# Optimization experiments

Measured on AMD Instinct MI355X. Metric: run time of the kernel, lower is better.

The kernel has to match this reference:

```python
import jax, jax.numpy as jnp
import numpy as np

EPS = 1.1920929e-07  # float32 eps, matches torch.finfo(torch.float32).eps
QMAX = 127.0         # 2**(8-1)-1 for 8-bit symmetric quantization
NUM_HEADS = 12


def _round_ste(x):
    return x + jax.lax.stop_gradient(jnp.round(x) - x)


def _floor_ste(x):
    return x + jax.lax.stop_gradient(jnp.floor(x) - x)


def _act_quant(x):
    # per-tensor symmetric 8-bit (QuantAct + SymmetricQuantFunction)
    s = jax.lax.stop_gradient(jnp.maximum(jnp.max(jnp.abs(x)) / QMAX, EPS))
    return jnp.clip(_round_ste(x / s), -QMAX - 1.0, QMAX), s


def _weight_quant(w):
    # per-output-channel symmetric 8-bit (scale.view(-1,1) path in linear_quantize)
    s = jax.lax.stop_gradient(jnp.maximum(jnp.max(jnp.abs(w), axis=1) / QMAX, EPS))
    return jnp.clip(_round_ste(w / s[:, None]), -QMAX - 1.0, QMAX), s


def _fixedpoint_requant(pre_act, pre_s, z_s):
    # fixedpoint_mul: requantize int accumulator (value pre_act on scale pre_s)
    # onto scale z_s using a 31-bit mantissa/exponent decomposition (batch_frexp).
    def int_path(pa):
        z_int = jnp.round(pa / pre_s)
        ns = pre_s / z_s
        e = jnp.floor(jnp.log2(ns)) + 1.0          # frexp exponent: ns = m * 2**e, m in [0.5,1)
        m = jnp.floor(ns * jnp.exp2(-e) * 2.0 ** 31 + 0.5)  # ROUND_HALF_UP mantissa * 2**31
        out = jnp.round(z_int * m * jnp.exp2(e - 31.0))
        return jnp.clip(out, -QMAX - 1.0, QMAX)
    hard = jax.lax.stop_gradient(int_path(pre_act))
    soft = pre_act / z_s                            # STE backward: grad / z_scaling_factor
    return soft + jax.lax.stop_gradient(hard - soft)


def _int_softmax(x_int, sf, output_bit=8, n=15):
    # IntSoftmax (shiftmax) with int_exp_shift; x_int = logits / sf (integer-valued)
    x_int = x_int - jnp.max(x_int, axis=-1, keepdims=True)
    x_int = x_int + _floor_ste(x_int / 2.0) - _floor_ste(x_int / 16.0)
    x0 = jax.lax.stop_gradient(jnp.floor(-1.0 / sf))
    x_int = jnp.maximum(x_int, n * x0)
    q = _floor_ste(x_int / x0)
    r = x_int - x0 * q
    exp_int = jnp.clip(_floor_ste((r / 2.0 - x0) * jnp.exp2(n - q)), 0.0, None)
    esum = jnp.minimum(jnp.sum(exp_int, axis=-1, keepdims=True), 2.0 ** 31 - 1.0)
    factor = _floor_ste((2.0 ** 31 - 1.0) / esum)
    exp_int = _floor_ste(exp_int * factor / 2.0 ** (31 - output_bit + 1))
    return exp_int, 1.0 / 2.0 ** (output_bit - 1)


def setup_inputs() -> dict:
    key = jax.random.key(0)
    k1, k2, k3, k4, k5 = jax.random.split(key, 5)
    B, N, C = 8, 577, 768
    return {
        "x": jax.random.normal(k1, (B, N, C), dtype=jnp.float32),
        "w_qkv": jax.random.normal(k2, (3 * C, C), dtype=jnp.float32) * 0.02,
        "b_qkv": jax.random.normal(k3, (3 * C,), dtype=jnp.float32) * 0.01,
        "w_proj": jax.random.normal(k4, (C, C), dtype=jnp.float32) * 0.02,
        "b_proj": jax.random.normal(k5, (C,), dtype=jnp.float32) * 0.01,
    }


def reference(x, w_qkv, b_qkv, w_proj, b_proj):
    B, N, C = x.shape
    H = NUM_HEADS
    D = C // H
    # ---- quantize input activation and qkv weight, integer GEMM ----
    x_int, s_x = _act_quant(x)                         # [B,N,C] int-valued, scalar scale
    wq_int, s_wq = _weight_quant(w_qkv)                # [3C,C], per-channel scale [3C]
    acc_s = s_x * s_wq                                 # accumulator scale [3C]
    qkv_int = jnp.einsum('bnc,oc->bno', x_int, wq_int) + _round_ste(b_qkv / acc_s)
    qkv_f = qkv_int * acc_s                            # dequantized qkv [B,N,3C]
    # ---- requantize qkv to per-tensor 8-bit via fixed-point mul ----
    s_qkv = jax.lax.stop_gradient(jnp.maximum(jnp.max(jnp.abs(qkv_f)) / QMAX, EPS))
    qkv8 = _fixedpoint_requant(qkv_f, acc_s, s_qkv)    # int8-valued [B,N,3C]
    qkv8 = qkv8.reshape(B, N, 3, H, D).transpose(2, 0, 3, 1, 4)
    q, k, v = qkv8[0], qkv8[1], qkv8[2]                # each [B,H,N,D]
    # ---- integer attention logits; float scale carries head_dim**-0.5 ----
    attn_int = jnp.einsum('bhnd,bhmd->bhnm', q, k)
    s_attn = s_qkv * s_qkv * (D ** -0.5)
    sm_int, s_sm = _int_softmax(attn_int, s_attn)      # int probs on scale 1/128
    # ---- integer attn @ v ----
    ctx_int = jnp.einsum('bhnm,bhmd->bhnd', sm_int, v)
    ctx_f = (ctx_int * (s_sm * s_qkv)).transpose(0, 2, 1, 3).reshape(B, N, C)
    s_ctx = jax.lax.stop_gradient(jnp.maximum(jnp.max(jnp.abs(ctx_f)) / QMAX, EPS))
    ctx8 = _fixedpoint_requant(ctx_f, s_sm * s_qkv, s_ctx)
    # ---- quantized output projection ----
    wp_int, s_wp = _weight_quant(w_proj)
    out_s = s_ctx * s_wp
    out_int = jnp.einsum('bnc,oc->bno', ctx8, wp_int) + _round_ste(b_proj / out_s)
    return out_int * out_s
```

## Files before the change

### kernel.cpp

```cpp
#include <hip/hip_runtime.h>
#include <math.h>

#define BQ 8
#define SEQ 577
#define CH 768
#define NH 12
#define HD 64
#define M_ROWS (BQ * SEQ)
#define QKV_CH (3 * CH)
#define NX (M_ROWS * CH)
#define EPSF 1.1920929e-07f
#define F2P31 2147483648.0f

#define VT_ROW 640
#define P_STRIDE 688

#define NSLOT 64
#define SLOT_STRIDE 16

typedef __attribute__((ext_vector_type(4))) int i32x4;

__device__ __forceinline__ float slot_scale(const unsigned* __restrict__ s) {
  float m = 0.f;
#pragma unroll
  for (int i = 0; i < NSLOT; ++i) m = fmaxf(m, __uint_as_float(s[i * SLOT_STRIDE]));
  return fmaxf(m / 127.0f, EPSF);
}

__device__ __forceinline__ void mfma_gemm_core_lds(
    const signed char* __restrict__ A, const signed char* __restrict__ Bm,
    signed char* As, signed char* Bs,
    int arow0, int bcol0, int w, int lane, i32x4 acc[4][4]) {
  int c = lane & 15, q = lane >> 4;
  int lr = lane >> 2;
  int ksb = (lane & 3) << 4;
  const signed char* Aw = As + ((w & 1) << 12);
  const signed char* Bw = Bs + ((w >> 1) << 12);
  for (int k0 = 0; k0 < CH; k0 += 64) {
#pragma unroll
    for (int u = 0; u < 2; ++u) {
      int row = (w << 5) + (u << 4) + lr;
      __builtin_amdgcn_global_load_lds(
          (const __attribute__((address_space(1))) void*)(A + (size_t)(arow0 + row) * CH + k0 + ksb),
          (__attribute__((address_space(3))) void*)(As + (w << 11) + (u << 10)),
          16, 0, 0);
      __builtin_amdgcn_global_load_lds(
          (const __attribute__((address_space(1))) void*)(Bm + (size_t)(bcol0 + row) * CH + k0 + ksb),
          (__attribute__((address_space(3))) void*)(Bs + (w << 11) + (u << 10)),
          16, 0, 0);
    }
    __syncthreads();
    i32x4 af[4], bf[4];
#pragma unroll
    for (int i = 0; i < 4; ++i)
      af[i] = *(const i32x4*)(Aw + (((i << 4) + c) << 6) + (q << 4));
#pragma unroll
    for (int j = 0; j < 4; ++j)
      bf[j] = *(const i32x4*)(Bw + (((j << 4) + c) << 6) + (q << 4));
#pragma unroll
    for (int i = 0; i < 4; ++i)
#pragma unroll
      for (int j = 0; j < 4; ++j)
        acc[i][j] = __builtin_amdgcn_mfma_i32_16x16x64_i8(af[i], bf[j], acc[i][j], 0, 0, 0);
    __syncthreads();
  }
}

__global__ __launch_bounds__(256) void k_prep(
    const float* __restrict__ x, const float* __restrict__ w_qkv,
    const float* __restrict__ w_proj,
    signed char* __restrict__ WQ8, float* __restrict__ SWQ,
    signed char* __restrict__ WP8, float* __restrict__ SWP,
    unsigned* __restrict__ mxx) {
  __shared__ float red[4];
  int blk = blockIdx.x, tid = threadIdx.x;
  if (blk < QKV_CH + CH) {
    const float* wr; signed char* w8; float* sw; int r;
    if (blk < QKV_CH) { r = blk; wr = w_qkv + (size_t)r * CH; w8 = WQ8 + (size_t)r * CH; sw = SWQ; }
    else { r = blk - QKV_CH; wr = w_proj + (size_t)r * CH; w8 = WP8 + (size_t)r * CH; sw = SWP; }
    const float4* wr4 = (const float4*)wr;
    float4 v = {0.f, 0.f, 0.f, 0.f};
    float m = 0.f;
    if (tid < CH / 4) {
      v = wr4[tid];
      m = fmaxf(fmaxf(fabsf(v.x), fabsf(v.y)), fmaxf(fabsf(v.z), fabsf(v.w)));
    }
#pragma unroll
    for (int o = 32; o; o >>= 1) m = fmaxf(m, __shfl_xor(m, o, 64));
    if ((tid & 63) == 0) red[tid >> 6] = m;
    __syncthreads();
    float mm = fmaxf(fmaxf(red[0], red[1]), fmaxf(red[2], red[3]));
    float s = fmaxf(mm / 127.0f, EPSF);
    if (tid == 0) sw[r] = s;
    if (tid < CH / 4) {
      int pk = 0;
#pragma unroll
      for (int u = 0; u < 4; ++u) {
        float xv = (u == 0) ? v.x : (u == 1) ? v.y : (u == 2) ? v.z : v.w;
        float q = rintf(xv / s);
        q = fminf(fmaxf(q, -128.f), 127.f);
        pk |= ((int)(signed char)q & 0xff) << (u * 8);
      }
      ((int*)w8)[tid] = pk;
    }
  } else {
    int ab = blk - (QKV_CH + CH);
    const float4* x4 = (const float4*)x;
    float m = 0.f;
    for (int i = ab * 256 + tid; i < NX / 4; i += 1024 * 256) {
      float4 v = x4[i];
      m = fmaxf(m, fmaxf(fmaxf(fabsf(v.x), fabsf(v.y)), fmaxf(fabsf(v.z), fabsf(v.w))));
    }
#pragma unroll
    for (int o = 32; o; o >>= 1) m = fmaxf(m, __shfl_xor(m, o, 64));
    if ((tid & 63) == 0) red[tid >> 6] = m;
    __syncthreads();
    if (tid == 0)
      atomicMax(&mxx[(ab & (NSLOT - 1)) * SLOT_STRIDE],
                __float_as_uint(fmaxf(fmaxf(red[0], red[1]), fmaxf(red[2], red[3]))));
  }
}

__global__ void k_aquant(const float* __restrict__ x, int n,
                         const unsigned* __restrict__ mxx, signed char* __restrict__ x8) {
  float s = slot_scale(mxx);
  int n4 = n >> 2;
  const float4* x4 = (const float4*)x;
  int* dst = (int*)x8;
  int stride = gridDim.x * blockDim.x;
  for (int i = blockIdx.x * blockDim.x + threadIdx.x; i < n4; i += stride) {
    float4 v = x4[i];
    int pk = 0;
#pragma unroll
    for (int u = 0; u < 4; ++u) {
      float xv = (u == 0) ? v.x : (u == 1) ? v.y : (u == 2) ? v.z : v.w;
      float q = rintf(xv / s);
      q = fminf(fmaxf(q, -128.f), 127.f);
      pk |= ((int)(signed char)q & 0xff) << (u * 8);
    }
    dst[i] = pk;
  }
}

__global__ __launch_bounds__(256) void k_gemm_qkv(
    const signed char* __restrict__ A, const signed char* __restrict__ Bm,
    const float* __restrict__ swq, const float* __restrict__ bias,
    const unsigned* __restrict__ mxx, int* __restrict__ Cq, unsigned* __restrict__ mxq) {
  __shared__ __align__(16) signed char As[8192], Bs[8192];
  __shared__ float red[4];
  int t = threadIdx.x;
  int lane = t & 63, w = t >> 6;
  int c = lane & 15, q = lane >> 4;
  int arow = blockIdx.y * 128 + (w & 1) * 64;
  int bcol = blockIdx.x * 128 + (w >> 1) * 64;
  i32x4 acc[4][4] = {};
  mfma_gemm_core_lds(A, Bm, As, Bs, blockIdx.y * 128, blockIdx.x * 128, w, lane, acc);
  float s_x = slot_scale(mxx);
  float lmax = 0.f;
#pragma unroll
  for (int j = 0; j < 4; ++j) {
    int ccol = bcol + j * 16 + c;
    float accs = s_x * swq[ccol];
    int bint = (int)rintf(bias[ccol] / accs);
#pragma unroll
    for (int i = 0; i < 4; ++i)
#pragma unroll
      for (int r = 0; r < 4; ++r) {
        int rr = arow + i * 16 + q * 4 + r;
        if (rr < M_ROWS) {
          int qv = acc[i][j][r] + bint;
          Cq[(size_t)rr * QKV_CH + ccol] = qv;
          lmax = fmaxf(lmax, fabsf((float)qv * accs));
        }
      }
  }
#pragma unroll
  for (int off = 32; off; off >>= 1) lmax = fmaxf(lmax, __shfl_xor(lmax, off, 64));
  if (lane == 0) red[w] = lmax;
  __syncthreads();
  if (t == 0)
    atomicMax(&mxq[((blockIdx.y * 18 + blockIdx.x) & (NSLOT - 1)) * SLOT_STRIDE],
              __float_as_uint(fmaxf(fmaxf(red[0], red[1]), fmaxf(red[2], red[3]))));
}

#define QK_BLKS 870
__global__ __launch_bounds__(256) void k_qkv_requant(
    const int* __restrict__ Cq, const float* __restrict__ swq,
    const unsigned* __restrict__ mxx, const unsigned* __restrict__ mxq,
    signed char* __restrict__ Q8, signed char* __restrict__ K8,
    signed char* __restrict__ VT8) {
  float s_x = slot_scale(mxx);
  float s_qkv = slot_scale(mxq);
  int blk = blockIdx.x, tid = threadIdx.x;
  if (blk < QK_BLKS) {
    int bx = blk % 6, by = blk / 6;
    int o = bx * 256 + tid;
    float accs = s_x * swq[o];
    float ns = accs / s_qkv;
    int e; float f = frexpf(ns, &e);
    float mm = floorf(f * F2P31 + 0.5f);
    float pw = __int_as_float((e + 96) << 23);
    int isK = (o >= CH);
    int rem = o - (isK ? CH : 0);
    int h = rem >> 6, d = rem & 63;
    signed char* dstb = isK ? K8 : Q8;
    int bn0 = by * 32;
    int bnend = min(bn0 + 32, M_ROWS);
    for (int bn = bn0; bn < bnend; ++bn) {
      int qv = Cq[(size_t)bn * QKV_CH + o];
      float qf = (float)qv * accs;
      float z = rintf(qf / accs);
      float t8 = rintf((z * mm) * pw);
      t8 = fminf(fmaxf(t8, -128.f), 127.f);
      int b = bn / SEQ, n = bn - b * SEQ;
      dstb[(((size_t)(b * NH + h) * SEQ + n) << 6) + d] = (signed char)t8;
    }
  } else {
    __shared__ __align__(16) signed char VTt[64 * 68];
    int vt = blk - QK_BLKS;
    int bh = vt / 10, n0 = (vt - bh * 10) * 64;
    int b = bh / NH, h = bh - b * NH;
    int od = tid & 63;
    int o = 2 * CH + h * 64 + od;
    float accs = s_x * swq[o];
    float ns = accs / s_qkv;
    int e; float f = frexpf(ns, &e);
    float mm = floorf(f * F2P31 + 0.5f);
    float pw = __int_as_float((e + 96) << 23);
    int nr = tid >> 6;
    for (int p = 0; p < 16; ++p) {
      int nl = nr * 16 + p;
      int n = n0 + nl;
      signed char v = 0;
      if (n < SEQ) {
        int qv = Cq[(size_t)(b * SEQ + n) * QKV_CH + o];
        float qf = (float)qv * accs;
        float z = rintf(qf / accs);
        float t8 = rintf((z * mm) * pw);
        t8 = fminf(fmaxf(t8, -128.f), 127.f);
        v = (signed char)t8;
      }
      VTt[od * 68 + nl] = v;
    }
    __syncthreads();
    int w16 = tid & 15, dr = tid >> 4;
#pragma unroll
    for (int pp = 0; pp < 4; ++pp) {
      int d = pp * 16 + dr;
      int val = *(const int*)&VTt[d * 68 + w16 * 4];
      *(int*)(VT8 + (size_t)bh * (64 * VT_ROW) + (size_t)d * VT_ROW + n0 + w16 * 4) = val;
    }
  }
}

__global__ __launch_bounds__(256, 6) void k_attn(
    const signed char* __restrict__ Q8, const signed char* __restrict__ K8,
    const signed char* __restrict__ VT8, const unsigned* __restrict__ mxq,
    int* __restrict__ ctxi, unsigned* __restrict__ mxc) {
  __shared__ __align__(16) unsigned char P[16 * P_STRIDE];
  __shared__ int Rmax[4][16];
  __shared__ unsigned long long Rsum[4][16];
  __shared__ float Rav[4];
  int tid = threadIdx.x;
  int t = tid & 63, wid = tid >> 6;
  int lin = blockIdx.x;
  int j = lin >> 3;
  int bh = (lin & 7) * 12 + j / 37;
  int qt = j % 37;
  int b = bh / NH, h = bh - b * NH;
  int col = t & 15, q4 = t >> 4;
  const signed char* Qb = Q8 + (((size_t)bh * SEQ + qt * 16 + col) << 6);
  i32x4 qa = *(const i32x4*)(Qb + q4 * 16);
  const signed char* Kb = K8 + ((size_t)bh * SEQ << 6);
  int kt0 = wid * 10;
  i32x4 sv[10];
  bool vld[10];
  int mx[4] = {-2147483647 - 1, -2147483647 - 1, -2147483647 - 1, -2147483647 - 1};
#pragma unroll
  for (int u = 0; u < 10; ++u) {
    int kt = kt0 + u;
    int krow = min(kt * 16 + col, SEQ - 1);
    const signed char* kr = Kb + ((size_t)krow << 6);
    i32x4 kb = *(const i32x4*)(kr + q4 * 16);
    i32x4 a = {0, 0, 0, 0};
    a = __builtin_amdgcn_mfma_i32_16x16x64_i8(qa, kb, a, 0, 0, 0);
    sv[u] = a;
    bool valid = (kt < 36) | ((kt == 36) & (col < 1));
    vld[u] = valid;
#pragma unroll
    for (int r = 0; r < 4; ++r)
      if (valid) mx[r] = max(mx[r], a[r]);
  }
#pragma unroll
  for (int r = 0; r < 4; ++r) {
    mx[r] = max(mx[r], __shfl_xor(mx[r], 1, 64));
    mx[r] = max(mx[r], __shfl_xor(mx[r], 2, 64));
    mx[r] = max(mx[r], __shfl_xor(mx[r], 4, 64));
    mx[r] = max(mx[r], __shfl_xor(mx[r], 8, 64));
  }
  if (col == 0) {
#pragma unroll
    for (int r = 0; r < 4; ++r) Rmax[wid][q4 * 4 + r] = mx[r];
  }
  __syncthreads();
#pragma unroll
  for (int r = 0; r < 4; ++r) {
    int row = q4 * 4 + r;
    mx[r] = max(max(Rmax[0][row], Rmax[1][row]), max(Rmax[2][row], Rmax[3][row]));
  }
  float s_qkv = slot_scale(mxq);
  float s_attn = (s_qkv * s_qkv) * 0.125f;
  float x0f = floorf(-1.0f / s_attn);
  int x0i = (int)x0f;
  int bi = -x0i;
  int nx0i = 15 * x0i;
  int twob = bi << 1;
  unsigned Mq = 0xFFFFFFFFu / (unsigned)bi + 1u;
  bool bOne = (Mq == 0u);
  unsigned long long su[4] = {0ull, 0ull, 0ull, 0ull};
#pragma unroll
  for (int u = 0; u < 10; ++u) {
#pragma unroll
    for (int r = 0; r < 4; ++r) {
      int d = sv[u][r] - mx[r];
      int xi = d + (d >> 1) - (d >> 4);
      xi = max(xi, nx0i);
      xi = min(xi, 0);
      unsigned a = (unsigned)(-xi);
      unsigned q = bOne ? a : __umulhi(a, Mq);
      int rr = (int)(a - q * (unsigned)bi);
      unsigned m = (unsigned)(twob - rr);
      unsigned ue = (m << 15) >> (q + 1);
      ue = vld[u] ? ue : 0u;
      su[r] += ue;
      sv[u][r] = (int)ue;
    }
  }
#pragma unroll
  for (int r = 0; r < 4; ++r) {
    su[r] += __shfl_xor(su[r], 1, 64);
    su[r] += __shfl_xor(su[r], 2, 64);
    su[r] += __shfl_xor(su[r], 4, 64);
    su[r] += __shfl_xor(su[r], 8, 64);
  }
  if (col == 0) {
#pragma unroll
    for (int r = 0; r < 4; ++r) Rsum[wid][q4 * 4 + r] = su[r];
  }
  __syncthreads();
  float facS[4];
#pragma unroll
  for (int r = 0; r < 4; ++r) {
    int row = q4 * 4 + r;
    unsigned long long dv = ((Rsum[0][row] + Rsum[1][row]) + Rsum[2][row]) + Rsum[3][row];
    float esum = fminf((float)dv, F2P31);
    facS[r] = floorf(F2P31 / esum) * 5.9604644775390625e-08f;
  }
#pragma unroll
  for (int u = 0; u < 10; ++u) {
    int kt = kt0 + u;
#pragma unroll
    for (int r = 0; r < 4; ++r) {
      float e = (float)(unsigned)sv[u][r];
      int p = (int)floorf(e * facS[r]);
      P[(q4 * 4 + r) * P_STRIDE + kt * 16 + col] = (unsigned char)p;
    }
  }
  __syncthreads();
  const signed char* Vb = VT8 + (size_t)bh * (64 * VT_ROW);
  i32x4 ac0 = {0, 0, 0, 0}, ac1 = {0, 0, 0, 0};
#pragma unroll
  for (int mc = 0; mc < 10; mc += 2) {
    i32x4 pa0 = *(const i32x4*)&P[col * P_STRIDE + mc * 64 + q4 * 16];
    i32x4 vb0 = *(const i32x4*)(Vb + (size_t)(wid * 16 + col) * VT_ROW + mc * 64 + q4 * 16);
    ac0 = __builtin_amdgcn_mfma_i32_16x16x64_i8(pa0, vb0, ac0, 0, 0, 0);
    i32x4 pa1 = *(const i32x4*)&P[col * P_STRIDE + (mc + 1) * 64 + q4 * 16];
    i32x4 vb1 = *(const i32x4*)(Vb + (size_t)(wid * 16 + col) * VT_ROW + (mc + 1) * 64 + q4 * 16);
    ac1 = __builtin_amdgcn_mfma_i32_16x16x64_i8(pa1, vb1, ac1, 0, 0, 0);
  }
  float pre_s = 0.0078125f * s_qkv;
  float avmax = 0.f;
#pragma unroll
  for (int r = 0; r < 4; ++r) {
    int n = qt * 16 + q4 * 4 + r;
    if (n < SEQ) {
      int cacc = ac0[r] + ac1[r];
      ctxi[((size_t)(b * SEQ + n)) * CH + h * 64 + wid * 16 + col] = cacc;
      avmax = fmaxf(avmax, fabsf((float)cacc * pre_s));
    }
  }
#pragma unroll
  for (int off = 32; off; off >>= 1) avmax = fmaxf(avmax, __shfl_xor(avmax, off, 64));
  if (t == 0) Rav[wid] = avmax;
  __syncthreads();
  if (tid == 0)
    atomicMax(&mxc[(blockIdx.x & (NSLOT - 1)) * SLOT_STRIDE],
              __float_as_uint(fmaxf(fmaxf(Rav[0], Rav[1]), fmaxf(Rav[2], Rav[3]))));
}

__global__ void k_ctx_requant(const int* __restrict__ ctxi, const unsigned* __restrict__ mxq,
                              const unsigned* __restrict__ mxc, signed char* __restrict__ C8) {
  float s_qkv = slot_scale(mxq);
  float pre_s = 0.0078125f * s_qkv;
  float s_ctx = slot_scale(mxc);
  float ns = pre_s / s_ctx;
  int e;
  float f = frexpf(ns, &e);
  float mm = floorf(f * F2P31 + 0.5f);
  float pw = exp2f((float)e - 31.0f);
  int total4 = (M_ROWS * CH) / 4;
  int stride = gridDim.x * blockDim.x;
  const int4* src = (const int4*)ctxi;
  int* dst = (int*)C8;
  for (int i = blockIdx.x * blockDim.x + threadIdx.x; i < total4; i += stride) {
    int4 v = src[i];
    int pk = 0;
#pragma unroll
    for (int u = 0; u < 4; ++u) {
      int cv = (u == 0) ? v.x : (u == 1) ? v.y : (u == 2) ? v.z : v.w;
      float cf = (float)cv * pre_s;
      float z = rintf(cf / pre_s);
      float t8 = rintf((z * mm) * pw);
      t8 = fminf(fmaxf(t8, -128.f), 127.f);
      pk |= ((int)(signed char)t8 & 0xff) << (u * 8);
    }
    dst[i] = pk;
  }
}

__global__ __launch_bounds__(256) void k_gemm_out(
    const signed char* __restrict__ A, const signed char* __restrict__ Bm,
    const float* __restrict__ swp, const float* __restrict__ bias,
    const unsigned* __restrict__ mxc, float* __restrict__ outp) {
  __shared__ __align__(16) signed char As[8192], Bs[8192];
  int t = threadIdx.x;
  int lane = t & 63, w = t >> 6;
  int c = lane & 15, q = lane >> 4;
  int arow = blockIdx.y * 128 + (w & 1) * 64;
  int bcol = blockIdx.x * 128 + (w >> 1) * 64;
  i32x4 acc[4][4] = {};
  mfma_gemm_core_lds(A, Bm, As, Bs, blockIdx.y * 128, blockIdx.x * 128, w, lane, acc);
  float s_ctx = slot_scale(mxc);
#pragma unroll
  for (int j = 0; j < 4; ++j) {
    int ccol = bcol + j * 16 + c;
    float outs = s_ctx * swp[ccol];
    int bint = (int)rintf(bias[ccol] / outs);
#pragma unroll
    for (int i = 0; i < 4; ++i)
#pragma unroll
      for (int r = 0; r < 4; ++r) {
        int rr = arow + i * 16 + q * 4 + r;
        if (rr < M_ROWS)
          outp[(size_t)rr * CH + ccol] = (float)(acc[i][j][r] + bint) * outs;
      }
  }
}

extern "C" void kernel_launch(void* const* d_in, const int* in_sizes, int n_in,
                              void* d_out, int out_size, void* d_ws, size_t ws_size,
                              hipStream_t stream) {
  const float* x = (const float*)d_in[0];
  const float* w_qkv = (const float*)d_in[1];
  const float* b_qkv = (const float*)d_in[2];
  const float* w_proj = (const float*)d_in[3];
  const float* b_proj = (const float*)d_in[4];
  float* outp = (float*)d_out;

  char* ws = (char*)d_ws;
  size_t off = 0;
  auto alloc = [&](size_t sz) -> char* {
    char* p = ws + off;
    off = (off + sz + 4095) & ~(size_t)4095;
    return p;
  };
  unsigned* mxx = (unsigned*)alloc(3 * NSLOT * SLOT_STRIDE * 4);
  unsigned* mxq = mxx + NSLOT * SLOT_STRIDE;
  unsigned* mxc = mxq + NSLOT * SLOT_STRIDE;
  float* SWQ = (float*)alloc(QKV_CH * 4);
  float* SWP = (float*)alloc(CH * 4);
  signed char* WQ8 = (signed char*)alloc((size_t)QKV_CH * CH);
  signed char* WP8 = (signed char*)alloc((size_t)CH * CH);
  signed char* X8  = (signed char*)alloc((size_t)(M_ROWS + 128) * CH);
  signed char* Q8  = (signed char*)alloc((size_t)M_ROWS * CH);
  signed char* K8  = (signed char*)alloc((size_t)M_ROWS * CH);
  signed char* VT8 = (signed char*)alloc((size_t)BQ * NH * 64 * VT_ROW);
  signed char* C8  = (signed char*)alloc((size_t)(M_ROWS + 128) * CH);
  int* QKVI = (int*)alloc((size_t)M_ROWS * QKV_CH * 4);
  int* CTXI = (int*)alloc((size_t)M_ROWS * CH * 4);
  (void)ws_size;

  hipMemsetAsync(mxx, 0, 3 * NSLOT * SLOT_STRIDE * 4, stream);
  k_prep<<<QKV_CH + CH + 1024, 256, 0, stream>>>(x, w_qkv, w_proj, WQ8, SWQ, WP8, SWP, mxx);
  k_aquant<<<2048, 256, 0, stream>>>(x, NX, mxx, X8);
  dim3 g1(QKV_CH / 128, (M_ROWS + 127) / 128);
  k_gemm_qkv<<<g1, 256, 0, stream>>>(X8, WQ8, SWQ, b_qkv, mxx, QKVI, mxq);
  k_qkv_requant<<<QK_BLKS + BQ * NH * 10, 256, 0, stream>>>(QKVI, SWQ, mxx, mxq, Q8, K8, VT8);
  k_attn<<<37 * BQ * NH, 256, 0, stream>>>(Q8, K8, VT8, mxq, CTXI, mxc);
  k_ctx_requant<<<1024, 256, 0, stream>>>(CTXI, mxq, mxc, C8);
  dim3 g2(CH / 128, (M_ROWS + 127) / 128);
  k_gemm_out<<<g2, 256, 0, stream>>>(C8, WP8, SWP, b_proj, mxc, outp);
}
```

Baseline: 232.9 us.

## Fuse context requantization into output-projection GEMM A-tile loading

Removes the standalone k_ctx_requant kernel and the int8 C8 buffer. The output GEMM now reads int32 context accumulators directly, requantizes them to int8 in registers and writes them into LDS, while weights are still loaded via global_load_lds. This saves one launch and one full write and reread of the int8 buffer, but the GEMM reads A tiles as int32 (4x the bytes), and each of the 6 column blocks repeats the requant arithmetic. It also lowers the k_attn launch-bounds occupancy hint from 6 to 4.

```diff
diff --git a/kernel.cpp b/kernel.cpp
--- a/kernel.cpp
+++ b/kernel.cpp
@@ -253,7 +253,7 @@
   }
 }
 
-__global__ __launch_bounds__(256, 6) void k_attn(
+__global__ __launch_bounds__(256, 4) void k_attn(
     const signed char* __restrict__ Q8, const signed char* __restrict__ K8,
     const signed char* __restrict__ VT8, const unsigned* __restrict__ mxq,
     int* __restrict__ ctxi, unsigned* __restrict__ mxc) {
@@ -398,8 +398,20 @@
               __float_as_uint(fmaxf(fmaxf(Rav[0], Rav[1]), fmaxf(Rav[2], Rav[3]))));
 }
 
-__global__ void k_ctx_requant(const int* __restrict__ ctxi, const unsigned* __restrict__ mxq,
-                              const unsigned* __restrict__ mxc, signed char* __restrict__ C8) {
+__global__ __launch_bounds__(256) void k_gemm_out(
+    const int* __restrict__ CTXI, const signed char* __restrict__ Bm,
+    const float* __restrict__ swp, const float* __restrict__ bias,
+    const unsigned* __restrict__ mxq, const unsigned* __restrict__ mxc,
+    float* __restrict__ outp) {
+  __shared__ __align__(16) signed char As[8192], Bs[8192];
+  int t = threadIdx.x;
+  int lane = t & 63, w = t >> 6;
+  int c = lane & 15, q = lane >> 4;
+  int lr = lane >> 2;
+  int ksb = (lane & 3) << 4;
+  int arow0 = blockIdx.y * 128, bcol0 = blockIdx.x * 128;
+  int arow = arow0 + (w & 1) * 64;
+  int bcol = bcol0 + (w >> 1) * 64;
   float s_qkv = slot_scale(mxq);
   float pre_s = 0.0078125f * s_qkv;
   float s_ctx = slot_scale(mxc);
@@ -408,39 +420,51 @@
   float f = frexpf(ns, &e);
   float mm = floorf(f * F2P31 + 0.5f);
   float pw = exp2f((float)e - 31.0f);
-  int total4 = (M_ROWS * CH) / 4;
-  int stride = gridDim.x * blockDim.x;
-  const int4* src = (const int4*)ctxi;
-  int* dst = (int*)C8;
-  for (int i = blockIdx.x * blockDim.x + threadIdx.x; i < total4; i += stride) {
-    int4 v = src[i];
-    int pk = 0;
-#pragma unroll
-    for (int u = 0; u < 4; ++u) {
-      int cv = (u == 0) ? v.x : (u == 1) ? v.y : (u == 2) ? v.z : v.w;
-      float cf = (float)cv * pre_s;
-      float z = rintf(cf / pre_s);
-      float t8 = rintf((z * mm) * pw);
-      t8 = fminf(fmaxf(t8, -128.f), 127.f);
-      pk |= ((int)(signed char)t8 & 0xff) << (u * 8);
-    }
-    dst[i] = pk;
-  }
-}
-
-__global__ __launch_bounds__(256) void k_gemm_out(
-    const signed char* __restrict__ A, const signed char* __restrict__ Bm,
-    const float* __restrict__ swp, const float* __restrict__ bias,
-    const unsigned* __restrict__ mxc, float* __restrict__ outp) {
-  __shared__ __align__(16) signed char As[8192], Bs[8192];
-  int t = threadIdx.x;
-  int lane = t & 63, w = t >> 6;
-  int c = lane & 15, q = lane >> 4;
-  int arow = blockIdx.y * 128 + (w & 1) * 64;
-  int bcol = blockIdx.x * 128 + (w >> 1) * 64;
+  const signed char* Aw = As + ((w & 1) << 12);
+  const signed char* Bw = Bs + ((w >> 1) << 12);
   i32x4 acc[4][4] = {};
-  mfma_gemm_core_lds(A, Bm, As, Bs, blockIdx.y * 128, blockIdx.x * 128, w, lane, acc);
-  float s_ctx = slot_scale(mxc);
+  for (int k0 = 0; k0 < CH; k0 += 64) {
+#pragma unroll
+    for (int u = 0; u < 2; ++u) {
+      int row = (w << 5) + (u << 4) + lr;
+      __builtin_amdgcn_global_load_lds(
+          (const __attribute__((address_space(1))) void*)(Bm + (size_t)(bcol0 + row) * CH + k0 + ksb),
+          (__attribute__((address_space(3))) void*)(Bs + (w << 11) + (u << 10)),
+          16, 0, 0);
+      const int4* src = (const int4*)(CTXI + (size_t)(arow0 + row) * CH + k0 + (lane & 3) * 16);
+      int pk[4];
+#pragma unroll
+      for (int g = 0; g < 4; ++g) {
+        int4 v = src[g];
+        int p = 0;
+#pragma unroll
+        for (int uu = 0; uu < 4; ++uu) {
+          int cv = (uu == 0) ? v.x : (uu == 1) ? v.y : (uu == 2) ? v.z : v.w;
+          float cf = (float)cv * pre_s;
+          float z = rintf(cf / pre_s);
+          float t8 = rintf((z * mm) * pw);
+          t8 = fminf(fmaxf(t8, -128.f), 127.f);
+          p |= ((int)(signed char)t8 & 0xff) << (uu * 8);
+        }
+        pk[g] = p;
+      }
+      *(i32x4*)(As + (w << 11) + (u << 10) + lane * 16) = *(const i32x4*)pk;
+    }
+    __syncthreads();
+    i32x4 af[4], bf[4];
+#pragma unroll
+    for (int i = 0; i < 4; ++i)
+      af[i] = *(const i32x4*)(Aw + (((i << 4) + c) << 6) + (q << 4));
+#pragma unroll
+    for (int j = 0; j < 4; ++j)
+      bf[j] = *(const i32x4*)(Bw + (((j << 4) + c) << 6) + (q << 4));
+#pragma unroll
+    for (int i = 0; i < 4; ++i)
+#pragma unroll
+      for (int j = 0; j < 4; ++j)
+        acc[i][j] = __builtin_amdgcn_mfma_i32_16x16x64_i8(af[i], bf[j], acc[i][j], 0, 0, 0);
+    __syncthreads();
+  }
 #pragma unroll
   for (int j = 0; j < 4; ++j) {
     int ccol = bcol + j * 16 + c;
@@ -485,9 +509,8 @@
   signed char* Q8  = (signed char*)alloc((size_t)M_ROWS * CH);
   signed char* K8  = (signed char*)alloc((size_t)M_ROWS * CH);
   signed char* VT8 = (signed char*)alloc((size_t)BQ * NH * 64 * VT_ROW);
-  signed char* C8  = (signed char*)alloc((size_t)(M_ROWS + 128) * CH);
   int* QKVI = (int*)alloc((size_t)M_ROWS * QKV_CH * 4);
-  int* CTXI = (int*)alloc((size_t)M_ROWS * CH * 4);
+  int* CTXI = (int*)alloc((size_t)(M_ROWS + 128) * CH * 4);
   (void)ws_size;
 
   hipMemsetAsync(mxx, 0, 3 * NSLOT * SLOT_STRIDE * 4, stream);
@@ -497,7 +520,6 @@
   k_gemm_qkv<<<g1, 256, 0, stream>>>(X8, WQ8, SWQ, b_qkv, mxx, QKVI, mxq);
   k_qkv_requant<<<QK_BLKS + BQ * NH * 10, 256, 0, stream>>>(QKVI, SWQ, mxx, mxq, Q8, K8, VT8);
   k_attn<<<37 * BQ * NH, 256, 0, stream>>>(Q8, K8, VT8, mxq, CTXI, mxc);
-  k_ctx_requant<<<1024, 256, 0, stream>>>(CTXI, mxq, mxc, C8);
   dim3 g2(CH / 128, (M_ROWS + 127) / 128);
-  k_gemm_out<<<g2, 256, 0, stream>>>(C8, WP8, SWP, b_proj, mxc, outp);
-}
+  k_gemm_out<<<g2, 256, 0, stream>>>(CTXI, WP8, SWP, b_proj, mxq, mxc, outp);
+}
```

Measured after the change: 214.3 us. -8.0%, faster.

## Halve output-projection GEMM tile width to 128x64 and relax attention launch bounds

Applied to the files above, without the earlier changes.

The output projection GEMM now uses 128x64 tiles with its own inline MFMA loop loading through global_load_lds, doubling the grid so the small M x 768 problem fills more compute units. The attention kernel's launch bounds drop from 6 to 4 waves per SIMD, giving the compiler more registers at the cost of fewer resident blocks. Smaller tiles mean less B-tile reuse per A load and more blocks re-reading A.

```diff
diff --git a/kernel.cpp b/kernel.cpp
--- a/kernel.cpp
+++ b/kernel.cpp
@@ -253,7 +253,7 @@
   }
 }
 
-__global__ __launch_bounds__(256, 6) void k_attn(
+__global__ __launch_bounds__(256, 4) void k_attn(
     const signed char* __restrict__ Q8, const signed char* __restrict__ K8,
     const signed char* __restrict__ VT8, const unsigned* __restrict__ mxq,
     int* __restrict__ ctxi, unsigned* __restrict__ mxc) {
@@ -432,17 +432,52 @@
     const signed char* __restrict__ A, const signed char* __restrict__ Bm,
     const float* __restrict__ swp, const float* __restrict__ bias,
     const unsigned* __restrict__ mxc, float* __restrict__ outp) {
-  __shared__ __align__(16) signed char As[8192], Bs[8192];
+  __shared__ __align__(16) signed char As[8192], Bs[4096];
   int t = threadIdx.x;
   int lane = t & 63, w = t >> 6;
   int c = lane & 15, q = lane >> 4;
-  int arow = blockIdx.y * 128 + (w & 1) * 64;
-  int bcol = blockIdx.x * 128 + (w >> 1) * 64;
-  i32x4 acc[4][4] = {};
-  mfma_gemm_core_lds(A, Bm, As, Bs, blockIdx.y * 128, blockIdx.x * 128, w, lane, acc);
+  int lr = lane >> 2;
+  int ksb = (lane & 3) << 4;
+  int arow0 = blockIdx.y * 128, bcol0 = blockIdx.x * 64;
+  int arow = arow0 + (w & 1) * 64;
+  int bcol = bcol0 + (w >> 1) * 32;
+  const signed char* Aw = As + ((w & 1) << 12);
+  const signed char* Bw = Bs + ((w >> 1) << 11);
+  i32x4 acc[4][2] = {};
+  for (int k0 = 0; k0 < CH; k0 += 64) {
+#pragma unroll
+    for (int u = 0; u < 2; ++u) {
+      int row = (w << 5) + (u << 4) + lr;
+      __builtin_amdgcn_global_load_lds(
+          (const __attribute__((address_space(1))) void*)(A + (size_t)(arow0 + row) * CH + k0 + ksb),
+          (__attribute__((address_space(3))) void*)(As + (w << 11) + (u << 10)),
+          16, 0, 0);
+    }
+    {
+      int row = (w << 4) + lr;
+      __builtin_amdgcn_global_load_lds(
+          (const __attribute__((address_space(1))) void*)(Bm + (size_t)(bcol0 + row) * CH + k0 + ksb),
+          (__attribute__((address_space(3))) void*)(Bs + (w << 10)),
+          16, 0, 0);
+    }
+    __syncthreads();
+    i32x4 af[4], bf[2];
+#pragma unroll
+    for (int i = 0; i < 4; ++i)
+      af[i] = *(const i32x4*)(Aw + (((i << 4) + c) << 6) + (q << 4));
+#pragma unroll
+    for (int j = 0; j < 2; ++j)
+      bf[j] = *(const i32x4*)(Bw + (((j << 4) + c) << 6) + (q << 4));
+#pragma unroll
+    for (int i = 0; i < 4; ++i)
+#pragma unroll
+      for (int j = 0; j < 2; ++j)
+        acc[i][j] = __builtin_amdgcn_mfma_i32_16x16x64_i8(af[i], bf[j], acc[i][j], 0, 0, 0);
+    __syncthreads();
+  }
   float s_ctx = slot_scale(mxc);
 #pragma unroll
-  for (int j = 0; j < 4; ++j) {
+  for (int j = 0; j < 2; ++j) {
     int ccol = bcol + j * 16 + c;
     float outs = s_ctx * swp[ccol];
     int bint = (int)rintf(bias[ccol] / outs);
@@ -498,6 +533,6 @@
   k_qkv_requant<<<QK_BLKS + BQ * NH * 10, 256, 0, stream>>>(QKVI, SWQ, mxx, mxq, Q8, K8, VT8);
   k_attn<<<37 * BQ * NH, 256, 0, stream>>>(Q8, K8, VT8, mxq, CTXI, mxc);
   k_ctx_requant<<<1024, 256, 0, stream>>>(CTXI, mxq, mxc, C8);
-  dim3 g2(CH / 128, (M_ROWS + 127) / 128);
+  dim3 g2(CH / 64, (M_ROWS + 127) / 128);
   k_gemm_out<<<g2, 256, 0, stream>>>(C8, WP8, SWP, b_proj, mxc, outp);
 }
```

After: 195.5 us. 1.19x faster.
